# Performance work log

Measured on AMD Instinct MI355X. Metric: run time of the kernel, lower is better.

Reference implementation:

```python
import jax, jax.numpy as jnp
import numpy as np

B, N, D = 2, 2048, 768
H = 12
HD = D // H
SCALE = HD ** -0.5
EPS = 1e-8


def exp0(v, c):
    # Poincare exponential map at origin: tanh(sqrt(c)||v||) * v / (sqrt(c)||v||)
    sc = jnp.sqrt(c)
    n = jnp.sqrt(jnp.sum(v * v, axis=-1, keepdims=True))
    n = jnp.maximum(n, EPS)
    return jnp.tanh(sc * n) * v / (sc * n)


def log0(x, c):
    # Poincare log map at origin: artanh(sqrt(c)||x||) * x / (sqrt(c)||x||)
    sc = jnp.sqrt(c)
    n = jnp.sqrt(jnp.sum(x * x, axis=-1, keepdims=True))
    n = jnp.maximum(n, EPS)
    t = jnp.clip(sc * n, 0.0, 1.0 - 1e-7)
    return jnp.arctanh(t) * x / (sc * n)


def setup_inputs() -> dict:
    key = jax.random.key(0)
    k1, k2, k3 = jax.random.split(key, 3)
    c0 = 0.1
    x = jax.random.normal(k1, (B, N, D), dtype=jnp.float32)
    # rescale so sqrt(c)*||x|| = 0.5 -> valid points strictly inside the ball
    xn = jnp.sqrt(jnp.sum(x * x, axis=-1, keepdims=True))
    x = x * (0.5 / (np.sqrt(c0) * jnp.maximum(xn, EPS)))
    w_qkv = jax.random.normal(k2, (3 * D, D), dtype=jnp.float32) * (D ** -0.5)
    w_proj = jax.random.normal(k3, (D, D), dtype=jnp.float32) * (D ** -0.5)
    b_proj = jnp.zeros((D,), dtype=jnp.float32)
    curvature = jnp.asarray(c0, dtype=jnp.float32)
    return {"x": x, "w_qkv": w_qkv, "w_proj": w_proj, "b_proj": b_proj,
            "curvature": curvature}


def reference(x, w_qkv, w_proj, b_proj, curvature):
    c = curvature
    v = log0(x, c)                                   # [B,N,D] tangent vectors
    qkv = jnp.einsum('bnd,ed->bne', v, w_qkv)        # [B,N,3D]
    qkv = qkv.reshape(B, N, 3, H, HD).transpose(2, 0, 3, 1, 4)  # [3,B,H,N,HD]
    q, k, v_proj = qkv[0], qkv[1], qkv[2]
    # Map q,k back onto the manifold for the hyperbolic distance score
    qm = exp0(q, c)                                  # [B,H,N,HD]
    km = exp0(k, c)
    q_nsq = jnp.sum(qm * qm, axis=-1)                # [B,H,N]
    k_nsq = jnp.sum(km * km, axis=-1)                # [B,H,N]
    dot = jnp.einsum('bhnd,bhmd->bhnm', qm, km)      # [B,H,N,N]
    # ||q-k||^2 = ||q||^2 + ||k||^2 - 2 q.k  (avoids [B,H,N,N,HD] intermediate)
    diff_sq = jnp.maximum(q_nsq[..., :, None] + k_nsq[..., None, :] - 2.0 * dot, 0.0)
    q_cl = jnp.minimum(q_nsq, 0.99)
    k_cl = jnp.minimum(k_nsq, 0.99)
    denom = (1.0 - q_cl)[..., :, None] * (1.0 - k_cl)[..., None, :] + 1e-8
    inner = jnp.maximum(1.0 + 2.0 * diff_sq / denom, 1.0 + 1e-7)
    distances = jnp.arccosh(inner)                   # [B,H,N,N]
    scores = -distances * SCALE
    attn = jax.nn.softmax(scores, axis=-1)
    out = jnp.einsum('bhnm,bhmd->bhnd', attn, v_proj)
    out = out.transpose(0, 2, 1, 3).reshape(B, N, D)
    v_out = jnp.einsum('bnd,ed->bne', out, w_proj) + b_proj
    return exp0(v_out, c)                            # [B,N,D] on manifold
```

## Files before the change

kernel.cpp:

```cpp
#include <hip/hip_runtime.h>
#include <cmath>

#define ROWS 4096
#define DIM 768
#define QKV_COLS 2304
#define NHEAD 12
#define HEAD_DIM 64
#define SEQ 2048

static constexpr float EPS_F = 1e-8f;

typedef __bf16 bfrag __attribute__((ext_vector_type(8)));
typedef float  f32x4 __attribute__((ext_vector_type(4)));
typedef float  f32x2 __attribute__((ext_vector_type(2)));

__device__ __forceinline__ float wave_sum64(float v) {
#pragma unroll
  for (int off = 1; off < 64; off <<= 1) v += __shfl_xor(v, off, 64);
  return v;
}

__device__ __forceinline__ unsigned short f2bf(float f) {
  unsigned u = __float_as_uint(f);
  u += 0x7fffu + ((u >> 16) & 1u);
  return (unsigned short)(u >> 16);
}

__device__ __forceinline__ float tanh_over_x(float x) {
  const float e  = __builtin_amdgcn_exp2f(x * 2.8853900817779268f);
  const float th = (e - 1.0f) * __builtin_amdgcn_rcpf(e + 1.0f);
  return (x < 1e-4f) ? 1.0f : th * __builtin_amdgcn_rcpf(x);
}

__device__ __forceinline__ void gl_lds16(const void* g, void* l) {
  __builtin_amdgcn_global_load_lds((const __attribute__((address_space(1))) void*)g,
                                   (__attribute__((address_space(3))) void*)l, 16, 0, 0);
}

__global__ __launch_bounds__(256) void log0_conv(const float* __restrict__ x,
                                                 const float* __restrict__ cptr,
                                                 unsigned short* __restrict__ vout,
                                                 const float* __restrict__ wa, int na,
                                                 const float* __restrict__ wb, int nb,
                                                 unsigned short* __restrict__ da,
                                                 unsigned short* __restrict__ db) {
  if (blockIdx.x >= ROWS / 4) {
    const int i = ((blockIdx.x - ROWS / 4) * 256 + threadIdx.x) * 4;
    const float* s;
    unsigned short* d;
    int j;
    if (i < na) { s = wa; d = da; j = i; }
    else { j = i - na; if (j >= nb) return; s = wb; d = db; }
    const float4 v = *(const float4*)(s + j);
    ushort4 o;
    o.x = f2bf(v.x); o.y = f2bf(v.y); o.z = f2bf(v.z); o.w = f2bf(v.w);
    *(ushort4*)(d + j) = o;
    return;
  }
  const int lane = threadIdx.x & 63;
  const int row  = (blockIdx.x << 2) + (threadIdx.x >> 6);
  const float* xr = x + (size_t)row * DIM;
  unsigned short* vr = vout + (size_t)row * DIM;
  float vals[12];
  float ss = 0.f;
#pragma unroll
  for (int i = 0; i < 12; ++i) {
    float t = xr[lane + (i << 6)];
    vals[i] = t;
    ss += t * t;
  }
  ss = wave_sum64(ss);
  const float sc  = sqrtf(cptr[0]);
  const float n   = fmaxf(sqrtf(ss), EPS_F);
  const float scn = sc * n;
  const float t   = fminf(scn, 1.0f - 1e-7f);
  const float ath = 0.34657359027997264f *
                    __builtin_amdgcn_logf((1.0f + t) * __builtin_amdgcn_rcpf(1.0f - t));
  const float f   = (scn < 1e-4f) ? 1.0f : ath * __builtin_amdgcn_rcpf(scn);
#pragma unroll
  for (int i = 0; i < 12; ++i) vr[lane + (i << 6)] = f2bf(vals[i] * f);
}

__global__ __launch_bounds__(256) void exp0_out_kernel(const float* __restrict__ vin,
                                                       const float* __restrict__ cptr,
                                                       float* __restrict__ outp) {
  const int lane = threadIdx.x & 63;
  const int row  = (blockIdx.x << 2) + (threadIdx.x >> 6);
  const float* vr = vin + (size_t)row * DIM;
  float* orow = outp + (size_t)row * DIM;
  float vals[12];
  float ss = 0.f;
#pragma unroll
  for (int i = 0; i < 12; ++i) {
    float t = vr[lane + (i << 6)];
    vals[i] = t;
    ss += t * t;
  }
  ss = wave_sum64(ss);
  const float sc = sqrtf(cptr[0]);
  const float n  = fmaxf(sqrtf(ss), EPS_F);
  const float f  = tanh_over_x(sc * n);
#pragma unroll
  for (int i = 0; i < 12; ++i) orow[lane + (i << 6)] = vals[i] * f;
}

template<int BM, int BN>
__global__ __launch_bounds__(256) void gemm_nt_dbuf(const unsigned short* __restrict__ A,
                                                    const unsigned short* __restrict__ B,
                                                    float* __restrict__ C,
                                                    int M, int Ncols, int K,
                                                    const float* __restrict__ bias) {
  constexpr int FI = BM / 32;
  constexpr int FJ = BN / 32;
  constexpr int CH = BM / 64;
  __shared__ unsigned short As[2][BM * 32];
  __shared__ unsigned short Bs[2][BN * 32];
  const int tid = threadIdx.x;
  const int w = tid >> 6, lane = tid & 63;
  const int lq = lane & 15, quad = lane >> 4;
  const int wr = w >> 1, wc = w & 1;
  const int row0 = blockIdx.y * BM;
  const int col0 = blockIdx.x * BN;
  const int srow  = lane >> 2;
  const int skoff = (lane & 3) << 3;

  f32x4 acc[FI][FJ];
#pragma unroll
  for (int i = 0; i < FI; ++i)
#pragma unroll
    for (int j = 0; j < FJ; ++j) acc[i][j] = (f32x4){0.f, 0.f, 0.f, 0.f};

  auto pf = [&](int k0, int buf) {
#pragma unroll
    for (int c = 0; c < CH; ++c) {
      const int r = c * 64 + w * 16;
      gl_lds16(A + (size_t)(row0 + r + srow) * K + k0 + skoff, &As[buf][r * 32]);
      gl_lds16(B + (size_t)(col0 + r + srow) * K + k0 + skoff, &Bs[buf][r * 32]);
    }
  };

  pf(0, 0);
  const int NIT = K / 32;
  for (int it = 0; it < NIT; ++it) {
    const int buf = it & 1;
    __syncthreads();
    if (it + 1 < NIT) pf((it + 1) * 32, buf ^ 1);

    bfrag af[FI], bfg[FJ];
#pragma unroll
    for (int i = 0; i < FI; ++i)
      af[i] = *(const bfrag*)&As[buf][(wr * (BM / 2) + i * 16 + lq) * 32 + (quad << 3)];
#pragma unroll
    for (int j = 0; j < FJ; ++j)
      bfg[j] = *(const bfrag*)&Bs[buf][(wc * (BN / 2) + j * 16 + lq) * 32 + (quad << 3)];
#pragma unroll
    for (int i = 0; i < FI; ++i)
#pragma unroll
      for (int j = 0; j < FJ; ++j)
        acc[i][j] = __builtin_amdgcn_mfma_f32_16x16x32_bf16(af[i], bfg[j], acc[i][j], 0, 0, 0);
  }

#pragma unroll
  for (int i = 0; i < FI; ++i) {
    const int crow = row0 + wr * (BM / 2) + i * 16 + (quad << 2);
#pragma unroll
    for (int j = 0; j < FJ; ++j) {
      const int col = col0 + wc * (BN / 2) + j * 16 + lq;
      const float bj = bias ? bias[col] : 0.0f;
      float* cp = C + (size_t)crow * Ncols + col;
#pragma unroll
      for (int r = 0; r < 4; ++r)
        cp[(size_t)r * Ncols] = acc[i][j][r] + bj;
    }
  }
}

__global__ __launch_bounds__(256) void gemm_qkv_fused(const unsigned short* __restrict__ A,
                                                      const unsigned short* __restrict__ B,
                                                      const float* __restrict__ cptr,
                                                      unsigned short* __restrict__ qh,
                                                      unsigned short* __restrict__ kh,
                                                      unsigned short* __restrict__ vth,
                                                      float* __restrict__ qnA,
                                                      float* __restrict__ qnB,
                                                      float* __restrict__ knA,
                                                      float* __restrict__ knB) {
  __shared__ unsigned short As[2][128 * 32];
  __shared__ unsigned short Bs[2][128 * 32];
  const int tid = threadIdx.x;
  const int w = tid >> 6, lane = tid & 63;
  const int lq = lane & 15, quad = lane >> 4;
  const int wr = w >> 1, wc = w & 1;
  const int row0 = blockIdx.y << 7;
  const int col0 = blockIdx.x << 7;
  const int srow  = lane >> 2;
  const int skoff = (lane & 3) << 3;

  f32x4 acc[4][4];
#pragma unroll
  for (int i = 0; i < 4; ++i)
#pragma unroll
    for (int j = 0; j < 4; ++j) acc[i][j] = (f32x4){0.f, 0.f, 0.f, 0.f};

  auto pf = [&](int k0, int buf) {
#pragma unroll
    for (int c = 0; c < 2; ++c) {
      const int r = c * 64 + w * 16;
      gl_lds16(A + (size_t)(row0 + r + srow) * DIM + k0 + skoff, &As[buf][r * 32]);
      gl_lds16(B + (size_t)(col0 + r + srow) * DIM + k0 + skoff, &Bs[buf][r * 32]);
    }
  };

  pf(0, 0);
  for (int it = 0; it < DIM / 32; ++it) {
    const int buf = it & 1;
    __syncthreads();
    if (it + 1 < DIM / 32) pf((it + 1) * 32, buf ^ 1);

    bfrag af[4], bfg[4];
#pragma unroll
    for (int i = 0; i < 4; ++i)
      af[i] = *(const bfrag*)&As[buf][((wr << 6) + (i << 4) + lq) * 32 + (quad << 3)];
#pragma unroll
    for (int j = 0; j < 4; ++j)
      bfg[j] = *(const bfrag*)&Bs[buf][((wc << 6) + (j << 4) + lq) * 32 + (quad << 3)];
#pragma unroll
    for (int i = 0; i < 4; ++i)
#pragma unroll
      for (int j = 0; j < 4; ++j)
        acc[i][j] = __builtin_amdgcn_mfma_f32_16x16x32_bf16(af[i], bfg[j], acc[i][j], 0, 0, 0);
  }

  const int colw = col0 + (wc << 6);
  const int seg  = colw / DIM;
  const int hh   = (colw % DIM) >> 6;
  const int rowb = row0 + (wr << 6);

  if (seg == 2) {
#pragma unroll
    for (int i = 0; i < 4; ++i)
#pragma unroll
      for (int r = 0; r < 4; ++r) {
        const int rowg = rowb + (i << 4) + (quad << 2) + r;
        const int bh = (rowg >> 11) * NHEAD + hh;
        const int n_ = rowg & 2047;
#pragma unroll
        for (int j = 0; j < 4; ++j)
          vth[((size_t)bh * HEAD_DIM + (j << 4) + lq) * SEQ + n_] = f2bf(acc[i][j][r]);
      }
  } else {
    unsigned short* dst = seg ? kh : qh;
    float* nA = seg ? knA : qnA;
    float* nB = seg ? knB : qnB;
    const float sc = sqrtf(cptr[0]);
#pragma unroll
    for (int i = 0; i < 4; ++i)
#pragma unroll
      for (int r = 0; r < 4; ++r) {
        float ss = acc[i][0][r] * acc[i][0][r];
        ss = fmaf(acc[i][1][r], acc[i][1][r], ss);
        ss = fmaf(acc[i][2][r], acc[i][2][r], ss);
        ss = fmaf(acc[i][3][r], acc[i][3][r], ss);
        ss += __shfl_xor(ss, 1, 64);
        ss += __shfl_xor(ss, 2, 64);
        ss += __shfl_xor(ss, 4, 64);
        ss += __shfl_xor(ss, 8, 64);
        const float nn = fmaxf(sqrtf(ss), EPS_F);
        const float f  = tanh_over_x(sc * nn);
        const int rowg = rowb + (i << 4) + (quad << 2) + r;
        const int bh = (rowg >> 11) * NHEAD + hh;
        const int n_ = rowg & 2047;
        unsigned short* rp = dst + ((size_t)bh * SEQ + n_) * HEAD_DIM;
#pragma unroll
        for (int j = 0; j < 4; ++j)
          rp[(j << 4) + lq] = f2bf(acc[i][j][r] * f);
        if (lq == 0) {
          const float nrm = ss * f * f;
          nA[(size_t)bh * SEQ + n_] = nrm;
          nB[(size_t)bh * SEQ + n_] = 1.0f / (1.0f - fminf(nrm, 0.99f));
        }
      }
  }
}

__global__ __launch_bounds__(512, 6) void flash_mfma(const unsigned short* __restrict__ qh,
                                                     const unsigned short* __restrict__ kh,
                                                     const unsigned short* __restrict__ vth,
                                                     const float* __restrict__ qnA,
                                                     const float* __restrict__ qnB,
                                                     const float* __restrict__ knA,
                                                     const float* __restrict__ knB,
                                                     unsigned short* __restrict__ attn_out) {
  const int flat = blockIdx.x;
  const int bhid = flat % 24;
  const int qt   = flat / 24;
  const int h = bhid % NHEAD, b = bhid / NHEAD;
  const int bh = b * NHEAD + h;
  const int tid = threadIdx.x;
  const int w = tid >> 6, lane = tid & 63;
  const int lq = lane & 15, quad = lane >> 4;
  const int wq = w & 3;
  const int wh = w >> 2;

  __shared__ __align__(16) unsigned short Ks[2][2][32 * 64];
  __shared__ __align__(16) unsigned short Vt[2][2][64 * 32];
  __shared__ __align__(16) unsigned short Ps[8][16 * 32];

  const unsigned short* qbase = qh + ((size_t)bh * SEQ + (size_t)qt * 64) * HEAD_DIM;
  const float* knAb = knA + (size_t)bh * SEQ;
  const float* knBb = knB + (size_t)bh * SEQ;
  const char* khb = (const char*)(kh + (size_t)bh * SEQ * HEAD_DIM);
  const char* vtb = (const char*)(vth + (size_t)bh * HEAD_DIM * SEQ);

  const int krow = lane >> 3;
  const int koff = ((wq << 3) + krow) * 128 + (((lane & 7) ^ krow) << 4);
  const int c     = (wq << 6) + lane;
  const int vrow2 = c >> 3;
  const int vd    = (vrow2 << 1) + ((c >> 2) & 1);
  const int vg    = (c & 3) ^ (vrow2 & 3);
  const size_t voffb = (size_t)vd * (SEQ * 2);

  auto prefetch = [&](int kt, int buf) {
    const int kb = (wh << 10) + (kt << 5);
    gl_lds16(khb + (size_t)kb * 128 + koff, (char*)&Ks[wh][buf][0] + (wq << 10));
    gl_lds16(vtb + voffb + (size_t)(kb + (vg << 3)) * 2, (char*)&Vt[wh][buf][0] + (wq << 10));
  };

  bfrag aq[2];
#pragma unroll
  for (int khf = 0; khf < 2; ++khf)
    aq[khf] = *(const bfrag*)(qbase + (size_t)((wq << 4) + lq) * HEAD_DIM + khf * 32 + quad * 8);

  const float qnS = qnA[(size_t)bh * SEQ + qt * 64 + (wq << 4) + lq];
  const float rqS = 2.0f * qnB[(size_t)bh * SEQ + qt * 64 + (wq << 4) + lq];

  bfrag ones;
#pragma unroll
  for (int j = 0; j < 8; ++j) ones[j] = (__bf16)1.0f;

  f32x4 oacc[4];
  f32x4 lacc = (f32x4){0.f, 0.f, 0.f, 0.f};
#pragma unroll
  for (int d = 0; d < 4; ++d) oacc[d] = (f32x4){0.f, 0.f, 0.f, 0.f};
  const int swz = lq & 7;
  const int vsw = (lq >> 1) & 3;
  const int psx = ((lq >> 2) & 3) << 3;

  prefetch(0, 0);
  for (int kt = 0; kt < 32; ++kt) {
    const int buf = kt & 1;
    const int key0 = (wh << 10) + (kt << 5);
    __syncthreads();
    if (kt + 1 < 32) prefetch(kt + 1, buf ^ 1);

    f32x4 kna[2], knr[2];
#pragma unroll
    for (int st = 0; st < 2; ++st) {
      kna[st] = *(const f32x4*)(knAb + key0 + st * 16 + (quad << 2));
      knr[st] = *(const f32x4*)(knBb + key0 + st * 16 + (quad << 2));
    }

    f32x4 s[2];
#pragma unroll
    for (int st = 0; st < 2; ++st) s[st] = (f32x4){0.f, 0.f, 0.f, 0.f};
#pragma unroll
    for (int khf = 0; khf < 2; ++khf)
#pragma unroll
      for (int st = 0; st < 2; ++st) {
        const bfrag ak = *(const bfrag*)&Ks[wh][buf][(st * 16 + lq) * 64 + (((khf << 2) + quad) ^ swz) * 8];
        s[st] = __builtin_amdgcn_mfma_f32_16x16x32_bf16(ak, aq[khf], s[st], 0, 0, 0);
      }

#pragma unroll
    for (int st = 0; st < 2; ++st) {
      const f32x2 qn2 = (f32x2){qnS, qnS};
      const f32x2 m2  = (f32x2){-2.f, -2.f};
      const f32x2 one2 = (f32x2){1.f, 1.f};
      const f32x2 neg2 = (f32x2){-1.f, -1.f};
      const f32x2 zr2 = (f32x2){0.f, 0.f};

      f32x2 s_lo = (f32x2){s[st][0], s[st][1]};
      f32x2 s_hi = (f32x2){s[st][2], s[st][3]};
      f32x2 ka_lo = (f32x2){kna[st][0], kna[st][1]};
      f32x2 ka_hi = (f32x2){kna[st][2], kna[st][3]};
      f32x2 kr_lo = (f32x2){knr[st][0], knr[st][1]};
      f32x2 kr_hi = (f32x2){knr[st][2], knr[st][3]};

      f32x2 tt_lo = __builtin_elementwise_fma(m2, s_lo, qn2 + ka_lo);
      f32x2 tt_hi = __builtin_elementwise_fma(m2, s_hi, qn2 + ka_hi);
      tt_lo = __builtin_elementwise_max(tt_lo, zr2);
      tt_hi = __builtin_elementwise_max(tt_hi, zr2);
      f32x2 rr_lo = kr_lo * rqS;
      f32x2 rr_hi = kr_hi * rqS;
      f32x2 in_lo = __builtin_elementwise_fma(tt_lo, rr_lo, one2);
      f32x2 in_hi = __builtin_elementwise_fma(tt_hi, rr_hi, one2);
      f32x2 r2_lo = __builtin_elementwise_fma(in_lo, in_lo, neg2);
      f32x2 r2_hi = __builtin_elementwise_fma(in_hi, in_hi, neg2);
      f32x2 rt_lo = (f32x2){__builtin_amdgcn_sqrtf(r2_lo.x), __builtin_amdgcn_sqrtf(r2_lo.y)};
      f32x2 rt_hi = (f32x2){__builtin_amdgcn_sqrtf(r2_hi.x), __builtin_amdgcn_sqrtf(r2_hi.y)};
      f32x2 y_lo = in_lo + rt_lo;
      f32x2 y_hi = in_hi + rt_hi;

      unsigned u[4];
      u[0] = __float_as_uint(__builtin_amdgcn_exp2f(-0.125f * __builtin_amdgcn_logf(y_lo.x)));
      u[1] = __float_as_uint(__builtin_amdgcn_exp2f(-0.125f * __builtin_amdgcn_logf(y_lo.y)));
      u[2] = __float_as_uint(__builtin_amdgcn_exp2f(-0.125f * __builtin_amdgcn_logf(y_hi.x)));
      u[3] = __float_as_uint(__builtin_amdgcn_exp2f(-0.125f * __builtin_amdgcn_logf(y_hi.y)));
      uint2 pk;
      pk.x = __builtin_amdgcn_perm(u[1], u[0], 0x07060302u);
      pk.y = __builtin_amdgcn_perm(u[3], u[2], 0x07060302u);
      *(uint2*)&Ps[w][(lq << 5) + (((st << 4) + (quad << 2)) ^ psx)] = pk;
    }

    const bfrag ap = *(const bfrag*)&Ps[w][(lq << 5) + ((quad << 3) ^ psx)];
    lacc = __builtin_amdgcn_mfma_f32_16x16x32_bf16(ap, ones, lacc, 0, 0, 0);
#pragma unroll
    for (int d = 0; d < 4; ++d) {
      const int dd = (d << 4) + lq;
      const bfrag bv = *(const bfrag*)&Vt[wh][buf][(dd >> 1) * 64 + (dd & 1) * 32 + (quad ^ vsw) * 8];
      oacc[d] = __builtin_amdgcn_mfma_f32_16x16x32_bf16(ap, bv, oacc[d], 0, 0, 0);
    }
  }

  __syncthreads();
  float* cb = (float*)&Ks[0][0][0];
  float* lb = (float*)&Vt[0][0][0];
  const int ci = (wq << 6) + lane;
  if (wh) {
    float* p = cb + ci * 16;
#pragma unroll
    for (int d = 0; d < 4; ++d) *(f32x4*)(p + (d << 2)) = oacc[d];
    *(f32x4*)(lb + (ci << 2)) = lacc;
  }
  __syncthreads();
  if (wh) return;

  {
    const float* p = cb + ci * 16;
#pragma unroll
    for (int d = 0; d < 4; ++d) oacc[d] += *(const f32x4*)(p + (d << 2));
    lacc += *(const f32x4*)(lb + (ci << 2));
  }

  float rl4[4];
#pragma unroll
  for (int i = 0; i < 4; ++i) rl4[i] = __builtin_amdgcn_rcpf(lacc[i]);

  unsigned short* ob = attn_out + ((size_t)b * SEQ + (size_t)qt * 64 + (wq << 4)) * DIM + h * HEAD_DIM;
#pragma unroll
  for (int d = 0; d < 4; ++d)
#pragma unroll
    for (int i = 0; i < 4; ++i)
      ob[(size_t)(quad * 4 + i) * DIM + d * 16 + lq] = f2bf(oacc[d][i] * rl4[i]);
}

extern "C" void kernel_launch(void* const* d_in, const int* in_sizes, int n_in,
                              void* d_out, int out_size, void* d_ws, size_t ws_size,
                              hipStream_t stream) {
  const float* x      = (const float*)d_in[0];
  const float* w_qkv  = (const float*)d_in[1];
  const float* w_proj = (const float*)d_in[2];
  const float* b_proj = (const float*)d_in[3];
  const float* curv   = (const float*)d_in[4];
  float* outp = (float*)d_out;

  float* ws = (float*)d_ws;
  unsigned short* v_tan_bf = (unsigned short*)ws;
  unsigned short* attn_bf  = (unsigned short*)ws;
  float* v_out = ws + 1572864;
  unsigned short* qh  = (unsigned short*)(v_out + 3145728);
  unsigned short* kh  = qh + 3145728;
  unsigned short* vth = kh + 3145728;
  unsigned short* wqkv_bf  = vth + 3145728;
  unsigned short* wproj_bf = wqkv_bf + 1769472;
  float* qnA = (float*)(wproj_bf + 589824);
  float* qnB = qnA + 49152;
  float* knA = qnB + 49152;
  float* knB = knA + 49152;

  log0_conv<<<dim3(ROWS / 4 + 2304), dim3(256), 0, stream>>>(
      x, curv, v_tan_bf, w_qkv, 1769472, w_proj, 589824, wqkv_bf, wproj_bf);
  gemm_qkv_fused<<<dim3(QKV_COLS / 128, ROWS / 128), dim3(256), 0, stream>>>(
      v_tan_bf, wqkv_bf, curv, qh, kh, vth, qnA, qnB, knA, knB);
  flash_mfma<<<dim3(768), dim3(512), 0, stream>>>(qh, kh, vth, qnA, qnB, knA, knB, attn_bf);
  gemm_nt_dbuf<64, 64><<<dim3(DIM / 64, ROWS / 64), dim3(256), 0, stream>>>(
      attn_bf, wproj_bf, v_out, ROWS, DIM, DIM, b_proj);
  exp0_out_kernel<<<dim3(ROWS / 4), dim3(256), 0, stream>>>(v_out, curv, outp);
}
```

Before: 198.0 us.

## Split attention keys across blocks with atomic accumulation and separate normalize kernel

The attention kernel now splits the key range four ways across separate 256-thread blocks, so there are more, smaller blocks. It no longer reduces two wave halves inside one block through shared memory. Partial numerators and denominators are added with float atomics into zeroed fp32 buffers, and a new kernel normalizes them and writes bf16 for the projection GEMM. This aims to raise occupancy and parallelism. The cost is two memsets, heavy atomic traffic, an extra kernel launch and a larger fp32 round trip through memory.

```diff
diff --git a/kernel.cpp b/kernel.cpp
--- a/kernel.cpp
+++ b/kernel.cpp
@@ -102,6 +102,23 @@
   const float f  = tanh_over_x(sc * n);
 #pragma unroll
   for (int i = 0; i < 12; ++i) orow[lane + (i << 6)] = vals[i] * f;
+}
+
+__global__ __launch_bounds__(256) void norm_out(const float* __restrict__ o_acc,
+                                                const float* __restrict__ l_acc,
+                                                unsigned short* __restrict__ attn) {
+  const int lane = threadIdx.x & 63;
+  const int row  = (blockIdx.x << 2) + (threadIdx.x >> 6);
+  const int b = row >> 11, n = row & 2047;
+  unsigned short* orow = attn + (size_t)row * DIM;
+  const float* ob = o_acc + ((size_t)(b * NHEAD) * SEQ + n) * 64;
+#pragma unroll
+  for (int h = 0; h < NHEAD; ++h) {
+    const float l = l_acc[(size_t)(b * NHEAD + h) * SEQ + n];
+    const float r = __builtin_amdgcn_rcpf(l);
+    const float v = ob[(size_t)h * SEQ * 64 + lane];
+    orow[(h << 6) + lane] = f2bf(v * r);
+  }
 }
 
 template<int BM, int BN>
@@ -283,28 +300,27 @@
   }
 }
 
-__global__ __launch_bounds__(512, 6) void flash_mfma(const unsigned short* __restrict__ qh,
+__global__ __launch_bounds__(256, 8) void flash_mfma(const unsigned short* __restrict__ qh,
                                                      const unsigned short* __restrict__ kh,
                                                      const unsigned short* __restrict__ vth,
                                                      const float* __restrict__ qnA,
                                                      const float* __restrict__ qnB,
                                                      const float* __restrict__ knA,
                                                      const float* __restrict__ knB,
-                                                     unsigned short* __restrict__ attn_out) {
+                                                     float* __restrict__ o_acc,
+                                                     float* __restrict__ l_acc) {
   const int flat = blockIdx.x;
-  const int bhid = flat % 24;
-  const int qt   = flat / 24;
-  const int h = bhid % NHEAD, b = bhid / NHEAD;
-  const int bh = b * NHEAD + h;
+  const int bhks = flat % 96;
+  const int qt   = flat / 96;
+  const int bh   = bhks % 24;
+  const int ks   = bhks / 24;
   const int tid = threadIdx.x;
   const int w = tid >> 6, lane = tid & 63;
   const int lq = lane & 15, quad = lane >> 4;
-  const int wq = w & 3;
-  const int wh = w >> 2;
-
-  __shared__ __align__(16) unsigned short Ks[2][2][32 * 64];
-  __shared__ __align__(16) unsigned short Vt[2][2][64 * 32];
-  __shared__ __align__(16) unsigned short Ps[8][16 * 32];
+
+  __shared__ __align__(16) unsigned short Ks[2][32 * 64];
+  __shared__ __align__(16) unsigned short Vt[2][64 * 32];
+  __shared__ __align__(16) unsigned short Ps[4][16 * 32];
 
   const unsigned short* qbase = qh + ((size_t)bh * SEQ + (size_t)qt * 64) * HEAD_DIM;
   const float* knAb = knA + (size_t)bh * SEQ;
@@ -313,26 +329,26 @@
   const char* vtb = (const char*)(vth + (size_t)bh * HEAD_DIM * SEQ);
 
   const int krow = lane >> 3;
-  const int koff = ((wq << 3) + krow) * 128 + (((lane & 7) ^ krow) << 4);
-  const int c     = (wq << 6) + lane;
+  const int koff = ((w << 3) + krow) * 128 + (((lane & 7) ^ krow) << 4);
+  const int c     = (w << 6) + lane;
   const int vrow2 = c >> 3;
   const int vd    = (vrow2 << 1) + ((c >> 2) & 1);
   const int vg    = (c & 3) ^ (vrow2 & 3);
   const size_t voffb = (size_t)vd * (SEQ * 2);
 
   auto prefetch = [&](int kt, int buf) {
-    const int kb = (wh << 10) + (kt << 5);
-    gl_lds16(khb + (size_t)kb * 128 + koff, (char*)&Ks[wh][buf][0] + (wq << 10));
-    gl_lds16(vtb + voffb + (size_t)(kb + (vg << 3)) * 2, (char*)&Vt[wh][buf][0] + (wq << 10));
+    const int kb = (ks << 9) + (kt << 5);
+    gl_lds16(khb + (size_t)kb * 128 + koff, (char*)&Ks[buf][0] + (w << 10));
+    gl_lds16(vtb + voffb + (size_t)(kb + (vg << 3)) * 2, (char*)&Vt[buf][0] + (w << 10));
   };
 
   bfrag aq[2];
 #pragma unroll
   for (int khf = 0; khf < 2; ++khf)
-    aq[khf] = *(const bfrag*)(qbase + (size_t)((wq << 4) + lq) * HEAD_DIM + khf * 32 + quad * 8);
-
-  const float qnS = qnA[(size_t)bh * SEQ + qt * 64 + (wq << 4) + lq];
-  const float rqS = 2.0f * qnB[(size_t)bh * SEQ + qt * 64 + (wq << 4) + lq];
+    aq[khf] = *(const bfrag*)(qbase + (size_t)((w << 4) + lq) * HEAD_DIM + khf * 32 + quad * 8);
+
+  const float qnS = qnA[(size_t)bh * SEQ + qt * 64 + (w << 4) + lq];
+  const float rqS = 2.0f * qnB[(size_t)bh * SEQ + qt * 64 + (w << 4) + lq];
 
   bfrag ones;
 #pragma unroll
@@ -347,11 +363,11 @@
   const int psx = ((lq >> 2) & 3) << 3;
 
   prefetch(0, 0);
-  for (int kt = 0; kt < 32; ++kt) {
+  for (int kt = 0; kt < 16; ++kt) {
     const int buf = kt & 1;
-    const int key0 = (wh << 10) + (kt << 5);
+    const int key0 = (ks << 9) + (kt << 5);
     __syncthreads();
-    if (kt + 1 < 32) prefetch(kt + 1, buf ^ 1);
+    if (kt + 1 < 16) prefetch(kt + 1, buf ^ 1);
 
     f32x4 kna[2], knr[2];
 #pragma unroll
@@ -367,7 +383,7 @@
     for (int khf = 0; khf < 2; ++khf)
 #pragma unroll
       for (int st = 0; st < 2; ++st) {
-        const bfrag ak = *(const bfrag*)&Ks[wh][buf][(st * 16 + lq) * 64 + (((khf << 2) + quad) ^ swz) * 8];
+        const bfrag ak = *(const bfrag*)&Ks[buf][(st * 16 + lq) * 64 + (((khf << 2) + quad) ^ swz) * 8];
         s[st] = __builtin_amdgcn_mfma_f32_16x16x32_bf16(ak, aq[khf], s[st], 0, 0, 0);
       }
 
@@ -417,41 +433,22 @@
 #pragma unroll
     for (int d = 0; d < 4; ++d) {
       const int dd = (d << 4) + lq;
-      const bfrag bv = *(const bfrag*)&Vt[wh][buf][(dd >> 1) * 64 + (dd & 1) * 32 + (quad ^ vsw) * 8];
+      const bfrag bv = *(const bfrag*)&Vt[buf][(dd >> 1) * 64 + (dd & 1) * 32 + (quad ^ vsw) * 8];
       oacc[d] = __builtin_amdgcn_mfma_f32_16x16x32_bf16(ap, bv, oacc[d], 0, 0, 0);
     }
   }
 
-  __syncthreads();
-  float* cb = (float*)&Ks[0][0][0];
-  float* lb = (float*)&Vt[0][0][0];
-  const int ci = (wq << 6) + lane;
-  if (wh) {
-    float* p = cb + ci * 16;
-#pragma unroll
-    for (int d = 0; d < 4; ++d) *(f32x4*)(p + (d << 2)) = oacc[d];
-    *(f32x4*)(lb + (ci << 2)) = lacc;
-  }
-  __syncthreads();
-  if (wh) return;
-
-  {
-    const float* p = cb + ci * 16;
-#pragma unroll
-    for (int d = 0; d < 4; ++d) oacc[d] += *(const f32x4*)(p + (d << 2));
-    lacc += *(const f32x4*)(lb + (ci << 2));
-  }
-
-  float rl4[4];
-#pragma unroll
-  for (int i = 0; i < 4; ++i) rl4[i] = __builtin_amdgcn_rcpf(lacc[i]);
-
-  unsigned short* ob = attn_out + ((size_t)b * SEQ + (size_t)qt * 64 + (wq << 4)) * DIM + h * HEAD_DIM;
+  float* ob = o_acc + ((size_t)bh * SEQ + (size_t)qt * 64 + (w << 4)) * 64;
 #pragma unroll
   for (int d = 0; d < 4; ++d)
 #pragma unroll
     for (int i = 0; i < 4; ++i)
-      ob[(size_t)(quad * 4 + i) * DIM + d * 16 + lq] = f2bf(oacc[d][i] * rl4[i]);
+      atomicAdd(&ob[(size_t)((quad << 2) + i) * 64 + (d << 4) + lq], oacc[d][i]);
+  if (lq == 0) {
+#pragma unroll
+    for (int i = 0; i < 4; ++i)
+      atomicAdd(&l_acc[(size_t)bh * SEQ + qt * 64 + (w << 4) + (quad << 2) + i], lacc[i]);
+  }
 }
 
 extern "C" void kernel_launch(void* const* d_in, const int* in_sizes, int n_in,
@@ -466,8 +463,9 @@
 
   float* ws = (float*)d_ws;
   unsigned short* v_tan_bf = (unsigned short*)ws;
-  unsigned short* attn_bf  = (unsigned short*)ws;
+  float* l_acc = ws;
   float* v_out = ws + 1572864;
+  float* o_acc = v_out;
   unsigned short* qh  = (unsigned short*)(v_out + 3145728);
   unsigned short* kh  = qh + 3145728;
   unsigned short* vth = kh + 3145728;
@@ -477,12 +475,16 @@
   float* qnB = qnA + 49152;
   float* knA = qnB + 49152;
   float* knB = knA + 49152;
-
+  unsigned short* attn_bf = kh;
+
+  hipMemsetAsync(o_acc, 0, (size_t)3145728 * sizeof(float), stream);
   log0_conv<<<dim3(ROWS / 4 + 2304), dim3(256), 0, stream>>>(
       x, curv, v_tan_bf, w_qkv, 1769472, w_proj, 589824, wqkv_bf, wproj_bf);
   gemm_qkv_fused<<<dim3(QKV_COLS / 128, ROWS / 128), dim3(256), 0, stream>>>(
       v_tan_bf, wqkv_bf, curv, qh, kh, vth, qnA, qnB, knA, knB);
-  flash_mfma<<<dim3(768), dim3(512), 0, stream>>>(qh, kh, vth, qnA, qnB, knA, knB, attn_bf);
+  hipMemsetAsync(l_acc, 0, (size_t)49152 * sizeof(float), stream);
+  flash_mfma<<<dim3(3072), dim3(256), 0, stream>>>(qh, kh, vth, qnA, qnB, knA, knB, o_acc, l_acc);
+  norm_out<<<dim3(ROWS / 4), dim3(256), 0, stream>>>(o_acc, l_acc, attn_bf);
   gemm_nt_dbuf<64, 64><<<dim3(DIM / 64, ROWS / 64), dim3(256), 0, stream>>>(
       attn_bf, wproj_bf, v_out, ROWS, DIM, DIM, b_proj);
   exp0_out_kernel<<<dim3(ROWS / 4), dim3(256), 0, stream>>>(v_out, curv, outp);
```

Measured after the change: 233.6 us. 1.18x slower.

## Load K fragments straight from global into registers instead of staging in LDS

Applied to the files above, without the earlier changes.

The K tile is no longer copied into shared memory. Each wave now reads its K MFMA operands directly from global memory into registers, and the loads for the next key block are issued one iteration ahead. The aim is to cut LDS traffic and shared-memory footprint, which could allow higher occupancy, and to drop the LDS reads of K. The cost is that the four query-row waves each fetch the same K data redundantly through the cache hierarchy, and global latency must be covered by that single-iteration register prefetch. The epilogue reduction buffers are moved onto the Vt and Ps arrays to replace the removed Ks array.

```diff
diff --git a/kernel.cpp b/kernel.cpp
--- a/kernel.cpp
+++ b/kernel.cpp
@@ -302,18 +302,15 @@
   const int wq = w & 3;
   const int wh = w >> 2;
 
-  __shared__ __align__(16) unsigned short Ks[2][2][32 * 64];
   __shared__ __align__(16) unsigned short Vt[2][2][64 * 32];
   __shared__ __align__(16) unsigned short Ps[8][16 * 32];
 
   const unsigned short* qbase = qh + ((size_t)bh * SEQ + (size_t)qt * 64) * HEAD_DIM;
+  const unsigned short* kb_ = kh + (size_t)bh * SEQ * HEAD_DIM;
   const float* knAb = knA + (size_t)bh * SEQ;
   const float* knBb = knB + (size_t)bh * SEQ;
-  const char* khb = (const char*)(kh + (size_t)bh * SEQ * HEAD_DIM);
   const char* vtb = (const char*)(vth + (size_t)bh * HEAD_DIM * SEQ);
 
-  const int krow = lane >> 3;
-  const int koff = ((wq << 3) + krow) * 128 + (((lane & 7) ^ krow) << 4);
   const int c     = (wq << 6) + lane;
   const int vrow2 = c >> 3;
   const int vd    = (vrow2 << 1) + ((c >> 2) & 1);
@@ -322,7 +319,6 @@
 
   auto prefetch = [&](int kt, int buf) {
     const int kb = (wh << 10) + (kt << 5);
-    gl_lds16(khb + (size_t)kb * 128 + koff, (char*)&Ks[wh][buf][0] + (wq << 10));
     gl_lds16(vtb + voffb + (size_t)(kb + (vg << 3)) * 2, (char*)&Vt[wh][buf][0] + (wq << 10));
   };
 
@@ -342,9 +338,17 @@
   f32x4 lacc = (f32x4){0.f, 0.f, 0.f, 0.f};
 #pragma unroll
   for (int d = 0; d < 4; ++d) oacc[d] = (f32x4){0.f, 0.f, 0.f, 0.f};
-  const int swz = lq & 7;
   const int vsw = (lq >> 1) & 3;
   const int psx = ((lq >> 2) & 3) << 3;
+
+  const unsigned short* kfl = kb_ + (size_t)lq * HEAD_DIM + quad * 8;
+
+  bfrag kf[2][2];
+#pragma unroll
+  for (int khf = 0; khf < 2; ++khf)
+#pragma unroll
+    for (int st = 0; st < 2; ++st)
+      kf[khf][st] = *(const bfrag*)(kfl + (size_t)((wh << 10) + st * 16) * HEAD_DIM + khf * 32);
 
   prefetch(0, 0);
   for (int kt = 0; kt < 32; ++kt) {
@@ -366,10 +370,17 @@
 #pragma unroll
     for (int khf = 0; khf < 2; ++khf)
 #pragma unroll
-      for (int st = 0; st < 2; ++st) {
-        const bfrag ak = *(const bfrag*)&Ks[wh][buf][(st * 16 + lq) * 64 + (((khf << 2) + quad) ^ swz) * 8];
-        s[st] = __builtin_amdgcn_mfma_f32_16x16x32_bf16(ak, aq[khf], s[st], 0, 0, 0);
-      }
+      for (int st = 0; st < 2; ++st)
+        s[st] = __builtin_amdgcn_mfma_f32_16x16x32_bf16(kf[khf][st], aq[khf], s[st], 0, 0, 0);
+
+    if (kt + 1 < 32) {
+      const int keyN = key0 + 32;
+#pragma unroll
+      for (int khf = 0; khf < 2; ++khf)
+#pragma unroll
+        for (int st = 0; st < 2; ++st)
+          kf[khf][st] = *(const bfrag*)(kfl + (size_t)(keyN + st * 16) * HEAD_DIM + khf * 32);
+    }
 
 #pragma unroll
     for (int st = 0; st < 2; ++st) {
@@ -423,8 +434,8 @@
   }
 
   __syncthreads();
-  float* cb = (float*)&Ks[0][0][0];
-  float* lb = (float*)&Vt[0][0][0];
+  float* cb = (float*)&Vt[0][0][0];
+  float* lb = (float*)&Ps[0][0];
   const int ci = (wq << 6) + lane;
   if (wh) {
     float* p = cb + ci * 16;
```

Result: slower. 252.9 us (+27.7%).
